# Kernel tuning notes

Hardware: AMD Instinct MI355X
Metric: run time of the kernel (lower is better)

The kernel has to match this reference:

```python
import jax, jax.numpy as jnp
import numpy as np
from jax import lax


def _leaky(x):
    # LeakyReLU, negative_slope=0.1
    return jnp.where(x > 0, x, 0.1 * x)


def _conv(x, w, pad, groups=1):
    # NCHW / OIHW 2D conv, stride 1
    return lax.conv_general_dilated(
        x, w, (1, 1), [(pad, pad), (pad, pad)],
        dimension_numbers=("NCHW", "OIHW", "NCHW"),
        feature_group_count=groups)


def setup_inputs() -> dict:
    key = jax.random.key(0)
    ks = jax.random.split(key, 12)
    B, C, H, W = 16, 64, 256, 256
    KS = 3

    def nrm(k, shape, fan_in):
        return jax.random.normal(k, shape, jnp.float32) / np.float32(np.sqrt(fan_in))

    return {
        "x": jax.random.normal(ks[0], (B, C, H, W), jnp.float32),
        "t": jax.random.normal(ks[1], (B, 1, 1, 1), jnp.float32),
        # t_process: 1x1 convs (1->64, 64->64), no bias -> stored as matrices
        "tW1": nrm(ks[2], (C, 1), 1),
        "tW2": nrm(ks[3], (C, C), C),
        # f_process: two 3x3 convs 64->64 with bias
        "fW1": nrm(ks[4], (C, C, KS, KS), C * KS * KS),
        "fb1": jnp.zeros((C,), jnp.float32),
        "fW2": nrm(ks[5], (C, C, KS, KS), C * KS * KS),
        "fb2": jnp.zeros((C,), jnp.float32),
        # kernel branch: 1x1 convs (1->64, 64->64*9), no bias
        "kW1": nrm(ks[6], (C, 1), 1),
        "kW2": nrm(ks[7], (C * KS * KS, C), C),
        # conv33: 3x3 conv 64->64 with bias
        "cW": nrm(ks[8], (C, C, KS, KS), C * KS * KS),
        "cb": jnp.zeros((C,), jnp.float32),
    }


def reference(x, t, tW1, tW2, fW1, fb1, fW2, fb2, kW1, kW2, cW, cb):
    b, c, h, w = x.shape
    KS = 3

    # f_process: Conv3x3 -> LeakyReLU -> Conv3x3 -> LeakyReLU
    f = _leaky(_conv(x, fW1, 1) + fb1[None, :, None, None])
    f = _leaky(_conv(f, fW2, 1) + fb2[None, :, None, None])

    # t is (b,1,1,1); 1x1 convs on it are per-sample matmuls
    ts = t.reshape(b, 1)
    # t_process: Conv1x1 -> LeakyReLU -> Conv1x1 -> Sigmoid -> (b,c,1,1)
    mv = jax.nn.sigmoid(_leaky(ts @ tW1.T) @ tW2.T).reshape(b, c, 1, 1)

    # kernel branch: Conv1x1 -> LeakyReLU -> Conv1x1 -> LeakyReLU -> (b*c,1,3,3)
    kern = _leaky(_leaky(ts @ kW1.T) @ kW2.T).reshape(b * c, 1, KS, KS)

    # per-sample-channel dynamic depthwise conv: groups = b*c
    out = _conv(f.reshape(1, b * c, h, w), kern, (KS - 1) // 2,
                groups=b * c).reshape(b, c, h, w)

    # modulation gating + residual 3x3 conv
    return out * mv + _conv(x, cW, 1) + cb[None, :, None, None]
```

## Files before the change

kernel.cpp:

```cpp
#include <hip/hip_runtime.h>
#include <cstdint>

using short8  = __attribute__((ext_vector_type(8))) short;
using short4v = __attribute__((ext_vector_type(4))) short;
using f32x16  = __attribute__((ext_vector_type(16))) float;
using float4v = __attribute__((ext_vector_type(4))) float;
typedef unsigned short ushort_t;

#define CHUNK_ROW 520
#define CHUNK_SLOTS 1560
#define BUF_SLOTS 1632
#define XSHW (BUF_SLOTS * 8)
#define WSHW (20 * 512)
#define XB0 WSHW
#define DYN1 ((WSHW + XSHW) * 2)
#define WSHM (40 * 512)
#define XBM WSHM
#define DYN02 ((WSHM + XSHW) * 2)

__device__ __forceinline__ float lrelu(float x) { return x > 0.f ? x : 0.1f * x; }

__device__ __forceinline__ ushort_t f2bf(float f) {
    union { float f; unsigned u; } v; v.f = f;
    unsigned r = (v.u + 0x7FFFu + ((v.u >> 16) & 1u)) >> 16;
    return (ushort_t)r;
}
__device__ __forceinline__ float bf2f(ushort_t b) {
    union { unsigned u; float f; } v; v.u = ((unsigned)b) << 16; return v.f;
}

__device__ __forceinline__ void gload_lds16(const ushort_t* g, ushort_t* l) {
    __builtin_amdgcn_global_load_lds(
        (const __attribute__((address_space(1))) void*)g,
        (__attribute__((address_space(3))) void*)l, 16, 0, 0);
}

#define VMCNT(n) asm volatile("s_waitcnt vmcnt(" #n ")" ::: "memory")
#define RBAR() __builtin_amdgcn_s_barrier()
#define SCHED0() __builtin_amdgcn_sched_barrier(0)

__global__ void k_tiny(const float* __restrict__ t, const float* __restrict__ tW1,
                       const float* __restrict__ tW2, const float* __restrict__ kW1,
                       const float* __restrict__ kW2, float* __restrict__ ktr) {
    int b = blockIdx.x;
    int c = threadIdx.x;
    __shared__ float h1[64], g1[64];
    float ts = t[b];
    h1[c] = lrelu(ts * tW1[c]);
    g1[c] = lrelu(ts * kW1[c]);
    __syncthreads();
    float s = 0.f;
    for (int j = 0; j < 64; ++j) s = fmaf(tW2[c * 64 + j], h1[j], s);
    float mvv = 1.f / (1.f + expf(-s));
    for (int q = 0; q < 9; ++q) {
        float s2 = 0.f;
        for (int j = 0; j < 64; ++j) s2 = fmaf(kW2[(c * 9 + q) * 64 + j], g1[j], s2);
        ktr[b * 576 + q * 64 + c] = lrelu(s2) * mvv;
    }
}

__global__ void k_zrow(ushort_t* __restrict__ z) {
    int i = blockIdx.x * 256 + threadIdx.x;
    *(short8*)(z + (size_t)i * 8) = (short8)0;
}

__global__ void k_pack(const float* __restrict__ w1, const float* __restrict__ w2,
                       const float* __restrict__ w3, ushort_t* __restrict__ wpM,
                       ushort_t* __restrict__ wp2) {
    int idx = blockIdx.x * 256 + threadIdx.x;
    const int NM = 4 * 36 * 512;
    if (idx >= NM + 4 * 18 * 512) return;
    const float* W;
    ushort_t* dst;
    int chunk, row, e;
    if (idx < NM) {
        chunk = idx / (36 * 512);
        int rem = idx % (36 * 512);
        row = rem / 512;
        e = rem % 512;
        W = (row < 18) ? w1 : w3;
        dst = wpM + idx;
        row %= 18;
    } else {
        int i2 = idx - NM;
        chunk = i2 / (18 * 512);
        int rem = i2 % (18 * 512);
        row = rem / 512;
        e = rem % 512;
        W = w2;
        dst = wp2 + i2;
    }
    int lane = e >> 3, j = e & 7;
    int t = row >> 1, ct = row & 1;
    int co = ct * 32 + (lane & 31);
    int ci = chunk * 16 + (lane >> 5) * 8 + j;
    *dst = f2bf(W[(co * 64 + ci) * 9 + t]);
}

__global__ __launch_bounds__(256) void k_tr(const float* __restrict__ x,
                                            ushort_t* __restrict__ xbf) {
    __shared__ ushort_t tl[64][66];
    int bid = blockIdx.x;
    int h = bid & 255, b = bid >> 8;
    int t = threadIdx.x;
    int cb = t >> 6;
    int wl = t & 63;
    for (int wt = 0; wt < 4; ++wt) {
        __syncthreads();
#pragma unroll
        for (int cc = 0; cc < 16; ++cc) {
            int c = cc * 4 + cb;
            float v = x[(((size_t)(b * 64 + c)) << 16) + h * 256 + wt * 64 + wl];
            tl[c][wl] = f2bf(v);
        }
        __syncthreads();
        int g = t & 7, w2 = t >> 3;
#pragma unroll
        for (int half = 0; half < 2; ++half) {
            int w = w2 + half * 32;
            short8 v;
#pragma unroll
            for (int j = 0; j < 8; ++j) v[j] = (short)tl[g * 8 + j][w];
            *(short8*)(xbf + (((size_t)(b * 256 + h) * 256 + wt * 64 + w) * 64 + g * 8)) = v;
        }
    }
}

#define STAGE_X(chunk, xbase)                                                    \
    {                                                                            \
        _Pragma("unroll")                                                        \
        for (int i_ = 0; i_ < 7; ++i_) {                                         \
            int base_ = wv * 390 + i_ * 64;                                      \
            int S_ = base_ + lane;                                               \
            S_ = S_ < CHUNK_SLOTS ? S_ : CHUNK_SLOTS - 1;                        \
            int row_ = (S_ >= 2 * CHUNK_ROW) ? 2 : (S_ >= CHUNK_ROW ? 1 : 0);    \
            int rem_ = S_ - row_ * CHUNK_ROW;                                    \
            int mg_ = rem_ >> 3, sl_ = rem_ & 7;                                 \
            int sp_ = sl_ ^ (mg_ & 7);                                           \
            int p_ = mg_ * 4 + (sp_ >> 1), g_ = sp_ & 1;                         \
            int wsx_ = p_ - 1;                                                   \
            bool edge_ = (unsigned)wsx_ >= 256u;                                 \
            const ushort_t* rp_ = (row_ == 0) ? rb0 : (row_ == 1 ? rb1 : rb2);   \
            const ushort_t* src_ =                                               \
                edge_ ? zv : (rp_ + wsx_ * 64 + (chunk)*16 + g_ * 8);            \
            gload_lds16(src_, xs + (xbase) + (size_t)base_ * 8);                 \
        }                                                                        \
    }

#define STAGE_W(chunk)                                                           \
    {                                                                            \
        _Pragma("unroll")                                                        \
        for (int i_ = 0; i_ < 5; ++i_) {                                         \
            int row_ = wv * 5 + i_;                                              \
            int rc_ = row_ > 17 ? 17 : row_;                                     \
            gload_lds16(wp + (size_t)((chunk)*18 + rc_) * 512 + lane * 8,        \
                        xs + (size_t)row_ * 512);                                \
        }                                                                        \
    }

#define STAGE_WM(chunk)                                                          \
    {                                                                            \
        _Pragma("unroll")                                                        \
        for (int i_ = 0; i_ < 10; ++i_) {                                        \
            int row_ = wv * 10 + i_;                                             \
            int rc_ = row_ > 35 ? 35 : row_;                                     \
            gload_lds16(wpM + (size_t)((chunk)*36 + rc_) * 512 + lane * 8,       \
                        xs + (size_t)row_ * 512);                                \
        }                                                                        \
    }

#define COMPUTE(xbase)                                                           \
    {                                                                            \
        __builtin_amdgcn_s_setprio(1);                                           \
        _Pragma("unroll")                                                        \
        for (int t_ = 0; t_ < 9; ++t_) {                                         \
            short8 a0 = *(const short8*)(xs + (size_t)(t_ * 2) * 512 + lane * 8);\
            short8 a1 = *(const short8*)(xs + (size_t)(t_ * 2 + 1) * 512 + lane * 8); \
            const int dwx_ = t_ % 3, rr_ = t_ / 3;                               \
            _Pragma("unroll")                                                    \
            for (int pt_ = 0; pt_ < 2; ++pt_) {                                  \
                int p_ = pw0 + pt_ * 32 + l31 + dwx_;                            \
                int mg_ = p_ >> 2;                                               \
                int sl_ = ((p_ & 3) * 2 + lhi) ^ (mg_ & 7);                      \
                short8 bf = *(const short8*)(                                    \
                    xs + (xbase) + (size_t)(rr_ * CHUNK_ROW + mg_ * 8 + sl_) * 8);\
                acc[0][pt_] = __builtin_amdgcn_mfma_f32_32x32x16_bf16(           \
                    a0, bf, acc[0][pt_], 0, 0, 0);                               \
                acc[1][pt_] = __builtin_amdgcn_mfma_f32_32x32x16_bf16(           \
                    a1, bf, acc[1][pt_], 0, 0, 0);                               \
            }                                                                    \
        }                                                                        \
        __builtin_amdgcn_s_setprio(0);                                           \
    }

#define COMPUTE_M()                                                              \
    {                                                                            \
        __builtin_amdgcn_s_setprio(1);                                           \
        _Pragma("unroll")                                                        \
        for (int t_ = 0; t_ < 9; ++t_) {                                         \
            short8 a0 = *(const short8*)(xs + (size_t)(t_ * 2) * 512 + lane * 8);\
            short8 a1 = *(const short8*)(xs + (size_t)(t_ * 2 + 1) * 512 + lane * 8); \
            short8 c0 = *(const short8*)(xs + (size_t)(18 + t_ * 2) * 512 + lane * 8); \
            short8 c1 = *(const short8*)(xs + (size_t)(19 + t_ * 2) * 512 + lane * 8); \
            const int dwx_ = t_ % 3, rr_ = t_ / 3;                               \
            _Pragma("unroll")                                                    \
            for (int pt_ = 0; pt_ < 2; ++pt_) {                                  \
                int p_ = pw0 + pt_ * 32 + l31 + dwx_;                            \
                int mg_ = p_ >> 2;                                               \
                int sl_ = ((p_ & 3) * 2 + lhi) ^ (mg_ & 7);                      \
                short8 bf = *(const short8*)(                                    \
                    xs + XBM + (size_t)(rr_ * CHUNK_ROW + mg_ * 8 + sl_) * 8);   \
                accA[0][pt_] = __builtin_amdgcn_mfma_f32_32x32x16_bf16(          \
                    a0, bf, accA[0][pt_], 0, 0, 0);                              \
                accA[1][pt_] = __builtin_amdgcn_mfma_f32_32x32x16_bf16(          \
                    a1, bf, accA[1][pt_], 0, 0, 0);                              \
                accC[0][pt_] = __builtin_amdgcn_mfma_f32_32x32x16_bf16(          \
                    c0, bf, accC[0][pt_], 0, 0, 0);                              \
                accC[1][pt_] = __builtin_amdgcn_mfma_f32_32x32x16_bf16(          \
                    c1, bf, accC[1][pt_], 0, 0, 0);                              \
            }                                                                    \
        }                                                                        \
        __builtin_amdgcn_s_setprio(0);                                           \
    }

__global__ __launch_bounds__(256, 2) void k_conv02(
    const ushort_t* __restrict__ in, const ushort_t* __restrict__ zv,
    const ushort_t* __restrict__ wpM, const float* __restrict__ ba,
    const float* __restrict__ bc, ushort_t* __restrict__ f1out,
    float* __restrict__ cres) {
    extern __shared__ __align__(16) ushort_t xs[];
    const int tid = threadIdx.x;
    const int lane = tid & 63;
    const int wv = tid >> 6;
    const unsigned bid = blockIdx.x;
    const unsigned L = (bid & 7u) * 512u + (bid >> 3);
    const int h = L & 255, b = L >> 8;
    const int l31 = lane & 31, lhi = lane >> 5;
    const int pw0 = wv * 64;

    const ushort_t* rb0 = (h > 0)   ? in + ((size_t)(b * 256 + h - 1)) * 16384 : zv;
    const ushort_t* rb1 =             in + ((size_t)(b * 256 + h)) * 16384;
    const ushort_t* rb2 = (h < 255) ? in + ((size_t)(b * 256 + h + 1)) * 16384 : zv;

    f32x16 accA[2][2], accC[2][2];
#pragma unroll
    for (int a = 0; a < 2; ++a)
#pragma unroll
        for (int c = 0; c < 2; ++c) { accA[a][c] = (f32x16)0.0f; accC[a][c] = (f32x16)0.0f; }

#pragma unroll
    for (int ch = 0; ch < 4; ++ch) {
        STAGE_WM(ch);
        STAGE_X(ch, XBM);
        VMCNT(0);
        RBAR(); SCHED0();
        COMPUTE_M();
        RBAR();
    }

    const int co_b = 4 * lhi;
    {
        ushort_t* outb = f1out + ((size_t)(b * 256 + h)) * 16384;
#pragma unroll
        for (int ct = 0; ct < 2; ++ct)
#pragma unroll
            for (int pt = 0; pt < 2; ++pt) {
                int pix = pw0 + pt * 32 + l31;
                ushort_t* po = outb + (size_t)pix * 64 + ct * 32 + co_b;
#pragma unroll
                for (int q = 0; q < 4; ++q) {
                    float4v bv = *(const float4v*)(ba + ct * 32 + co_b + 8 * q);
                    short4v sv;
#pragma unroll
                    for (int m = 0; m < 4; ++m) {
                        float v = lrelu(accA[ct][pt][q * 4 + m] + bv[m]);
                        sv[m] = (short)f2bf(v);
                    }
                    *(short4v*)(po + 8 * q) = sv;
                }
            }
    }
    {
        float* pb = cres + (((size_t)b * 64) << 16) + h * 256;
#pragma unroll
        for (int ct = 0; ct < 2; ++ct)
#pragma unroll
            for (int pt = 0; pt < 2; ++pt) {
                int pix = pw0 + pt * 32 + l31;
#pragma unroll
                for (int q = 0; q < 4; ++q) {
                    float4v bv = *(const float4v*)(bc + ct * 32 + co_b + 8 * q);
#pragma unroll
                    for (int m = 0; m < 4; ++m) {
                        int c = ct * 32 + co_b + 8 * q + m;
                        pb[((size_t)c << 16) + pix] = accC[ct][pt][q * 4 + m] + bv[m];
                    }
                }
            }
    }
}

__global__ __launch_bounds__(256, 3) void k_conv1(
    const ushort_t* __restrict__ in, const ushort_t* __restrict__ zv,
    const ushort_t* __restrict__ wp, const float* __restrict__ bias,
    ushort_t* __restrict__ outp) {
    extern __shared__ __align__(16) ushort_t xs[];
    const int tid = threadIdx.x;
    const int lane = tid & 63;
    const int wv = tid >> 6;
    const unsigned bid = blockIdx.x;
    const unsigned L = (bid & 7u) * 512u + (bid >> 3);
    const int h = L & 255, b = L >> 8;
    const int l31 = lane & 31, lhi = lane >> 5;
    const int pw0 = wv * 64;

    const ushort_t* rb0 = (h > 0)   ? in + ((size_t)(b * 256 + h - 1)) * 16384 : zv;
    const ushort_t* rb1 =             in + ((size_t)(b * 256 + h)) * 16384;
    const ushort_t* rb2 = (h < 255) ? in + ((size_t)(b * 256 + h + 1)) * 16384 : zv;

    f32x16 acc[2][2];
#pragma unroll
    for (int a = 0; a < 2; ++a)
#pragma unroll
        for (int c = 0; c < 2; ++c) acc[a][c] = (f32x16)0.0f;

#pragma unroll
    for (int ch = 0; ch < 4; ++ch) {
        STAGE_W(ch);
        STAGE_X(ch, XB0);
        VMCNT(0);
        RBAR(); SCHED0();
        COMPUTE(XB0);
        RBAR();
    }

    const int co_b = 4 * lhi;
    ushort_t* pb = outp + (((size_t)b * 64) << 16) + h * 256;
#pragma unroll
    for (int ct = 0; ct < 2; ++ct)
#pragma unroll
        for (int pt = 0; pt < 2; ++pt) {
            int pix = pw0 + pt * 32 + l31;
#pragma unroll
            for (int q = 0; q < 4; ++q) {
                float4v bv = *(const float4v*)(bias + ct * 32 + co_b + 8 * q);
#pragma unroll
                for (int m = 0; m < 4; ++m) {
                    int c = ct * 32 + co_b + 8 * q + m;
                    float v = lrelu(acc[ct][pt][q * 4 + m] + bv[m]);
                    pb[((size_t)c << 16) + pix] = f2bf(v);
                }
            }
        }
}

__global__ __launch_bounds__(256) void k_fin(const ushort_t* __restrict__ f2,
                                             const float* __restrict__ ktr,
                                             float* __restrict__ out) {
    __shared__ __align__(16) ushort_t s[10 * 272];
    const unsigned bid = blockIdx.x;
    const unsigned L = (bid & 7u) * 4096u + (bid >> 3);
    const int hb = L & 31, c = (L >> 5) & 63, b = L >> 11;
    const int h0 = hb * 8;
    const int w = threadIdx.x;

    const ushort_t* f2c = f2 + (((size_t)(b * 64 + c)) << 16);
    for (int i = w; i < 320; i += 256) {
        int r = i >> 5, seg = i & 31;
        int hs = h0 - 1 + r;
        short8 v = (short8)0;
        if ((unsigned)hs < 256u) v = *(const short8*)(f2c + hs * 256 + seg * 8);
        *(short8*)(&s[r * 272 + 8 + seg * 8]) = v;
        if (seg == 0) s[r * 272 + 7] = 0;
        if (seg == 31) s[r * 272 + 264] = 0;
    }
    __syncthreads();

    float kv[9];
#pragma unroll
    for (int t9 = 0; t9 < 9; ++t9) kv[t9] = ktr[b * 576 + t9 * 64 + c];

    float lv[10], cv[10], rv[10];
#pragma unroll
    for (int r = 0; r < 10; ++r) {
        lv[r] = bf2f(s[r * 272 + 7 + w]);
        cv[r] = bf2f(s[r * 272 + 8 + w]);
        rv[r] = bf2f(s[r * 272 + 9 + w]);
    }

    float* ob = out + (((size_t)(b * 64 + c)) << 16) + h0 * 256 + w;
#pragma unroll
    for (int rr = 0; rr < 8; ++rr) {
        float dwv = 0.f;
#pragma unroll
        for (int r3 = 0; r3 < 3; ++r3) {
            dwv = fmaf(kv[r3 * 3 + 0], lv[rr + r3], dwv);
            dwv = fmaf(kv[r3 * 3 + 1], cv[rr + r3], dwv);
            dwv = fmaf(kv[r3 * 3 + 2], rv[rr + r3], dwv);
        }
        float* po = ob + rr * 256;
        *po = *po + dwv;
    }
}

extern "C" void kernel_launch(void* const* d_in, const int* in_sizes, int n_in,
                              void* d_out, int out_size, void* d_ws, size_t ws_size,
                              hipStream_t stream) {
    const float* x   = (const float*)d_in[0];
    const float* t   = (const float*)d_in[1];
    const float* tW1 = (const float*)d_in[2];
    const float* tW2 = (const float*)d_in[3];
    const float* fW1 = (const float*)d_in[4];
    const float* fb1 = (const float*)d_in[5];
    const float* fW2 = (const float*)d_in[6];
    const float* fb2 = (const float*)d_in[7];
    const float* kW1 = (const float*)d_in[8];
    const float* kW2 = (const float*)d_in[9];
    const float* cW  = (const float*)d_in[10];
    const float* cb  = (const float*)d_in[11];

    char* ws = (char*)d_ws;
    float*    ktr  = (float*)ws;
    ushort_t* wpM  = (ushort_t*)(ws + 65536);
    ushort_t* wp2  = wpM + 4 * 36 * 512;
    ushort_t* zv   = (ushort_t*)(ws + 294912);
    ushort_t* xbf  = (ushort_t*)(ws + (512u << 10));
    ushort_t* f1bf = (ushort_t*)(ws + (512u << 10) + ((size_t)128 << 20));
    ushort_t* f2n  = xbf;
    float*    out  = (float*)d_out;

    hipFuncSetAttribute(reinterpret_cast<const void*>(&k_conv02),
                        hipFuncAttributeMaxDynamicSharedMemorySize, DYN02);
    hipFuncSetAttribute(reinterpret_cast<const void*>(&k_conv1),
                        hipFuncAttributeMaxDynamicSharedMemorySize, DYN1);

    k_tiny<<<dim3(16), dim3(64), 0, stream>>>(t, tW1, tW2, kW1, kW2, ktr);
    k_zrow<<<dim3(8), dim3(256), 0, stream>>>(zv);
    k_pack<<<dim3((4 * 36 * 512 + 4 * 18 * 512 + 255) / 256), dim3(256), 0, stream>>>(
        fW1, fW2, cW, wpM, wp2);
    k_tr<<<dim3(4096), dim3(256), 0, stream>>>(x, xbf);

    k_conv02<<<dim3(4096), dim3(256), DYN02, stream>>>(
        xbf, zv, wpM, fb1, cb, f1bf, out);
    k_conv1<<<dim3(4096), dim3(256), DYN1, stream>>>(f1bf, zv, wp2, fb2, f2n);
    k_fin<<<dim3(32768), dim3(256), 0, stream>>>(f2n, ktr, out);
}
```

Baseline: 601.2 us.

## Double-buffer input staging in conv1 and merge setup kernels into one launch

k_conv1 now uses two LDS input buffers, so the load of the next input chunk overlaps the MFMA compute on the current one. It waits with a partial vmcnt instead of draining all loads before each chunk. The larger LDS footprint lowers the occupancy hint from 3 to 2 blocks per CU. Separately, the tiny modulation kernel, the zero-row kernel and the weight-pack kernel are merged into a single k_setup launch to cut launch overhead.

```diff
diff --git a/kernel.cpp b/kernel.cpp
--- a/kernel.cpp
+++ b/kernel.cpp
@@ -13,7 +13,8 @@
 #define XSHW (BUF_SLOTS * 8)
 #define WSHW (20 * 512)
 #define XB0 WSHW
-#define DYN1 ((WSHW + XSHW) * 2)
+#define XB1 (WSHW + XSHW)
+#define DYN1 ((WSHW + 2 * XSHW) * 2)
 #define WSHM (40 * 512)
 #define XBM WSHM
 #define DYN02 ((WSHM + XSHW) * 2)
@@ -39,62 +40,70 @@
 #define RBAR() __builtin_amdgcn_s_barrier()
 #define SCHED0() __builtin_amdgcn_sched_barrier(0)
 
-__global__ void k_tiny(const float* __restrict__ t, const float* __restrict__ tW1,
-                       const float* __restrict__ tW2, const float* __restrict__ kW1,
-                       const float* __restrict__ kW2, float* __restrict__ ktr) {
-    int b = blockIdx.x;
-    int c = threadIdx.x;
+__global__ __launch_bounds__(256) void k_setup(
+    const float* __restrict__ t, const float* __restrict__ tW1,
+    const float* __restrict__ tW2, const float* __restrict__ kW1,
+    const float* __restrict__ kW2, const float* __restrict__ w1,
+    const float* __restrict__ w2, const float* __restrict__ w3,
+    float* __restrict__ ktr, ushort_t* __restrict__ wpM,
+    ushort_t* __restrict__ wp2, ushort_t* __restrict__ zv) {
     __shared__ float h1[64], g1[64];
-    float ts = t[b];
-    h1[c] = lrelu(ts * tW1[c]);
-    g1[c] = lrelu(ts * kW1[c]);
-    __syncthreads();
-    float s = 0.f;
-    for (int j = 0; j < 64; ++j) s = fmaf(tW2[c * 64 + j], h1[j], s);
-    float mvv = 1.f / (1.f + expf(-s));
-    for (int q = 0; q < 9; ++q) {
-        float s2 = 0.f;
-        for (int j = 0; j < 64; ++j) s2 = fmaf(kW2[(c * 9 + q) * 64 + j], g1[j], s2);
-        ktr[b * 576 + q * 64 + c] = lrelu(s2) * mvv;
-    }
-}
-
-__global__ void k_zrow(ushort_t* __restrict__ z) {
-    int i = blockIdx.x * 256 + threadIdx.x;
-    *(short8*)(z + (size_t)i * 8) = (short8)0;
-}
-
-__global__ void k_pack(const float* __restrict__ w1, const float* __restrict__ w2,
-                       const float* __restrict__ w3, ushort_t* __restrict__ wpM,
-                       ushort_t* __restrict__ wp2) {
-    int idx = blockIdx.x * 256 + threadIdx.x;
-    const int NM = 4 * 36 * 512;
-    if (idx >= NM + 4 * 18 * 512) return;
-    const float* W;
-    ushort_t* dst;
-    int chunk, row, e;
-    if (idx < NM) {
-        chunk = idx / (36 * 512);
-        int rem = idx % (36 * 512);
-        row = rem / 512;
-        e = rem % 512;
-        W = (row < 18) ? w1 : w3;
-        dst = wpM + idx;
-        row %= 18;
+    const int bid = blockIdx.x;
+    const int tid = threadIdx.x;
+    if (bid < 432) {
+        int idx = bid * 256 + tid;
+        const int NM = 4 * 36 * 512;
+        if (idx < NM + 4 * 18 * 512) {
+            const float* W;
+            ushort_t* dst;
+            int chunk, row, e;
+            if (idx < NM) {
+                chunk = idx / (36 * 512);
+                int rem = idx % (36 * 512);
+                row = rem / 512;
+                e = rem % 512;
+                W = (row < 18) ? w1 : w3;
+                dst = wpM + idx;
+                row %= 18;
+            } else {
+                int i2 = idx - NM;
+                chunk = i2 / (18 * 512);
+                int rem = i2 % (18 * 512);
+                row = rem / 512;
+                e = rem % 512;
+                W = w2;
+                dst = wp2 + i2;
+            }
+            int lane = e >> 3, j = e & 7;
+            int tt = row >> 1, ct = row & 1;
+            int co = ct * 32 + (lane & 31);
+            int ci = chunk * 16 + (lane >> 5) * 8 + j;
+            *dst = f2bf(W[(co * 64 + ci) * 9 + tt]);
+        }
+    } else if (bid < 440) {
+        int i = (bid - 432) * 256 + tid;
+        *(short8*)(zv + (size_t)i * 8) = (short8)0;
     } else {
-        int i2 = idx - NM;
-        chunk = i2 / (18 * 512);
-        int rem = i2 % (18 * 512);
-        row = rem / 512;
-        e = rem % 512;
-        W = w2;
-        dst = wp2 + i2;
-    }
-    int lane = e >> 3, j = e & 7;
-    int t = row >> 1, ct = row & 1;
-    int co = ct * 32 + (lane & 31);
-    int ci = chunk * 16 + (lane >> 5) * 8 + j;
-    *dst = f2bf(W[(co * 64 + ci) * 9 + t]);
+        int b = bid - 440;
+        int c = tid;
+        if (tid < 64) {
+            float ts = t[b];
+            h1[c] = lrelu(ts * tW1[c]);
+            g1[c] = lrelu(ts * kW1[c]);
+        }
+        __syncthreads();
+        if (tid < 64) {
+            float s = 0.f;
+            for (int j = 0; j < 64; ++j) s = fmaf(tW2[c * 64 + j], h1[j], s);
+            float mvv = 1.f / (1.f + expf(-s));
+            for (int q = 0; q < 9; ++q) {
+                float s2 = 0.f;
+                for (int j = 0; j < 64; ++j)
+                    s2 = fmaf(kW2[(c * 9 + q) * 64 + j], g1[j], s2);
+                ktr[b * 576 + q * 64 + c] = lrelu(s2) * mvv;
+            }
+        }
+    }
 }
 
 __global__ __launch_bounds__(256) void k_tr(const float* __restrict__ x,
@@ -300,7 +309,7 @@
     }
 }
 
-__global__ __launch_bounds__(256, 3) void k_conv1(
+__global__ __launch_bounds__(256, 2) void k_conv1(
     const ushort_t* __restrict__ in, const ushort_t* __restrict__ zv,
     const ushort_t* __restrict__ wp, const float* __restrict__ bias,
     ushort_t* __restrict__ outp) {
@@ -324,15 +333,27 @@
 #pragma unroll
         for (int c = 0; c < 2; ++c) acc[a][c] = (f32x16)0.0f;
 
-#pragma unroll
-    for (int ch = 0; ch < 4; ++ch) {
-        STAGE_W(ch);
-        STAGE_X(ch, XB0);
-        VMCNT(0);
-        RBAR(); SCHED0();
-        COMPUTE(XB0);
-        RBAR();
-    }
+    STAGE_W(0);
+    STAGE_X(0, XB0);
+    STAGE_X(1, XB1);
+    VMCNT(7);
+    RBAR(); SCHED0();
+    COMPUTE(XB0);
+    RBAR();
+    STAGE_W(1); STAGE_X(2, XB0);
+    VMCNT(7);
+    RBAR(); SCHED0();
+    COMPUTE(XB1);
+    RBAR();
+    STAGE_W(2); STAGE_X(3, XB1);
+    VMCNT(7);
+    RBAR(); SCHED0();
+    COMPUTE(XB0);
+    RBAR();
+    STAGE_W(3);
+    VMCNT(0);
+    RBAR(); SCHED0();
+    COMPUTE(XB1);
 
     const int co_b = 4 * lhi;
     ushort_t* pb = outp + (((size_t)b * 64) << 16) + h * 256;
@@ -434,10 +455,8 @@
     hipFuncSetAttribute(reinterpret_cast<const void*>(&k_conv1),
                         hipFuncAttributeMaxDynamicSharedMemorySize, DYN1);
 
-    k_tiny<<<dim3(16), dim3(64), 0, stream>>>(t, tW1, tW2, kW1, kW2, ktr);
-    k_zrow<<<dim3(8), dim3(256), 0, stream>>>(zv);
-    k_pack<<<dim3((4 * 36 * 512 + 4 * 18 * 512 + 255) / 256), dim3(256), 0, stream>>>(
-        fW1, fW2, cW, wpM, wp2);
+    k_setup<<<dim3(456), dim3(256), 0, stream>>>(
+        t, tW1, tW2, kW1, kW2, fW1, fW2, cW, ktr, wpM, wp2, zv);
     k_tr<<<dim3(4096), dim3(256), 0, stream>>>(x, xbf);
 
     k_conv02<<<dim3(4096), dim3(256), DYN02, stream>>>(
```

Result: faster. 581.5 us (-3.3%).
